# Performance work log

Measured on AMD Instinct MI355X. Metric: run time of the kernel, lower is better.

The kernel has to match this reference:

```python
import jax, jax.numpy as jnp
import numpy as np

D_MODEL = 96
D_STATE = 16
D_INNER = 192   # expand * d_model
DT_RANK = 6     # ceil(96/16)
D_DEPTH_OUT = 1024  # (64/2)*(64/2)
BATCH, HH, WW = 2, 64, 64


def silu(v):
    return v * jax.nn.sigmoid(v)


def setup_inputs() -> dict:
    key = jax.random.key(0)
    ks = jax.random.split(key, 10)
    f = jnp.float32
    x = jax.random.normal(ks[0], (BATCH, HH, WW, D_MODEL), f)
    in_proj_w = jax.random.normal(ks[1], (2 * D_INNER, D_MODEL), f) * 0.02
    conv2d_w = jax.random.normal(ks[2], (D_INNER, 1, 3, 3), f) * 0.1  # depthwise, groups=D_INNER
    conv2d_b = jnp.zeros((D_INNER,), f)
    depth_conv_w = jax.random.normal(ks[3], (D_INNER, 1, 3, 3), f) * 0.1  # depthwise, stride 2
    depth_conv_b = jnp.zeros((D_INNER,), f)
    depth_fc_w = jax.random.normal(ks[4], (D_INNER, D_DEPTH_OUT), f) * 0.02
    depth_fc_b = jnp.zeros((D_INNER,), f)
    x_proj_w = jax.random.normal(ks[5], (DT_RANK + 2 * D_STATE, D_INNER), f) * 0.02
    dt_init_std = DT_RANK ** (-0.5)
    dt_projs_w = jax.random.uniform(ks[6], (D_INNER, DT_RANK), f, -dt_init_std, dt_init_std)
    # inverse-softplus of dt ~ U(log 1e-3, log 0.1)
    dt = jnp.exp(jax.random.uniform(ks[7], (D_INNER,), f) * (np.log(0.1) - np.log(0.001)) + np.log(0.001))
    dt = jnp.clip(dt, 1e-4, None)
    dt_projs_b = dt + jnp.log(-jnp.expm1(-dt))
    A_logs = jnp.log(jnp.tile(jnp.arange(1, D_STATE + 1, dtype=f)[None, :], (D_INNER, 1)))
    Ds = jnp.ones((D_INNER,), f)
    out_norm_w = jnp.ones((D_INNER,), f)
    out_norm_b = jnp.zeros((D_INNER,), f)
    out_proj_w = jax.random.normal(ks[8], (D_MODEL, D_INNER), f) * 0.02
    return dict(x=x, in_proj_w=in_proj_w, conv2d_w=conv2d_w, conv2d_b=conv2d_b,
                depth_conv_w=depth_conv_w, depth_conv_b=depth_conv_b,
                depth_fc_w=depth_fc_w, depth_fc_b=depth_fc_b, x_proj_w=x_proj_w,
                dt_projs_w=dt_projs_w, dt_projs_b=dt_projs_b, A_logs=A_logs, Ds=Ds,
                out_norm_w=out_norm_w, out_norm_b=out_norm_b, out_proj_w=out_proj_w)


def _selective_scan(u, delta, A, Bm, Cm, D, delta_bias):
    # u, delta: [B, D, L]; A: [D, N]; Bm, Cm: [B, N, L]; D: [D]; delta_bias: [D]
    delta = jax.nn.softplus(delta + delta_bias[None, :, None])
    dA = jnp.exp(jnp.einsum('bdl,dn->lbdn', delta, A))          # [L,B,D,N]
    dBu = jnp.einsum('bdl,bnl,bdl->lbdn', delta, Bm, u)          # [L,B,D,N]
    Ct = jnp.transpose(Cm, (2, 0, 1))                            # [L,B,N]
    h0 = jnp.zeros(dA.shape[1:], u.dtype)

    def step(h, inp):
        a, b, c = inp
        h = a * h + b                                            # S6 recurrence
        return h, jnp.einsum('bdn,bn->bd', h, c)

    _, ys = jax.lax.scan(step, h0, (dA, dBu, Ct))                # ys: [L,B,D]
    y = jnp.transpose(ys, (1, 2, 0))                             # [B,D,L]
    return y + D[None, :, None] * u


def _forward(x, in_proj_w, conv2d_w, conv2d_b, depth_conv_w, depth_conv_b,
             depth_fc_w, depth_fc_b, x_proj_w, dt_projs_w, dt_projs_b,
             A_logs, Ds, out_norm_w, out_norm_b, out_proj_w):
    B, H, W, _ = x.shape
    Di, N, R = D_INNER, D_STATE, DT_RANK
    dn = ('NCHW', 'OIHW', 'NCHW')
    xz = x @ in_proj_w.T
    x1, z = jnp.split(xz, 2, axis=-1)
    xc = jnp.transpose(x1, (0, 3, 1, 2))                         # [B,Di,H,W]
    xc = jax.lax.conv_general_dilated(xc, conv2d_w, (1, 1), [(1, 1), (1, 1)],
                                      dimension_numbers=dn, feature_group_count=Di)
    xc = silu(xc + conv2d_b[None, :, None, None])
    dxc = jax.lax.conv_general_dilated(xc, depth_conv_w, (2, 2), [(1, 1), (1, 1)],
                                       dimension_numbers=dn, feature_group_count=Di)
    dxc = dxc + depth_conv_b[None, :, None, None]                # [B,Di,H/2,W/2]
    dx = dxc.reshape(B, Di, -1)                                  # [B,Di,1024]
    dx = dx @ depth_fc_w.T + depth_fc_b                          # [B,Di,Di]
    dx = silu(jnp.transpose(dx, (0, 2, 1)))                      # [B,Di,CC], CC=Di
    L = H * W
    CC = dx.shape[-1]
    xs = jnp.concatenate([dx, xc.reshape(B, Di, L)], axis=-1)    # mode='head': [B,Di,LL]
    x_dbl = jnp.einsum('bdl,cd->bcl', xs, x_proj_w)
    dts, Bm, Cm = x_dbl[:, :R], x_dbl[:, R:R + N], x_dbl[:, R + N:]
    dts = jnp.einsum('brl,dr->bdl', dts, dt_projs_w)
    A = -jnp.exp(A_logs)
    y = _selective_scan(xs, dts, A, Bm, Cm, Ds, dt_projs_b)
    y = y[..., CC:]                                              # drop depth tokens (head mode)
    y = jnp.transpose(y, (0, 2, 1)).reshape(B, H, W, Di)
    mu = jnp.mean(y, axis=-1, keepdims=True)
    var = jnp.var(y, axis=-1, keepdims=True)
    y = (y - mu) * jax.lax.rsqrt(var + 1e-5) * out_norm_w + out_norm_b
    y = y * silu(z)
    return y @ out_proj_w.T


def reference(x, in_proj_w, conv2d_w, conv2d_b, depth_conv_w, depth_conv_b,
              depth_fc_w, depth_fc_b, x_proj_w, dt_projs_w, dt_projs_b,
              A_logs, Ds, out_norm_w, out_norm_b, out_proj_w):
    return _forward(x, in_proj_w, conv2d_w, conv2d_b, depth_conv_w, depth_conv_b,
                    depth_fc_w, depth_fc_b, x_proj_w, dt_projs_w, dt_projs_b,
                    A_logs, Ds, out_norm_w, out_norm_b, out_proj_w)
```

## Files before the change

kernel.cpp:

```cpp
#include <hip/hip_runtime.h>
#include <hip/hip_bf16.h>

typedef __hip_bfloat16 bf16;

#define BATCH 2
#define DM 96
#define DI 192
#define LSP 4096
#define LD 192
#define LTOT 4288
#define NST 16
#define RK 6
#define DFC 1024
#define CLEN 64
#define NCH 67
#define SCH 64
#define XR 16
#define NG  (BATCH * DI * NST)

__device__ __forceinline__ float silu_f(float x) { return x / (1.f + __expf(-x)); }
__device__ __forceinline__ float softplus_f(float x) { return x > 20.f ? x : log1pf(__expf(x)); }

__device__ __forceinline__ int is_f32(const void* alog) {
    return ((const unsigned int*)alog)[0] == 0u;
}
__device__ __forceinline__ float LDI(const void* p, int i, int f32m) {
    return f32m ? ((const float*)p)[i] : __bfloat162float(((const bf16*)p)[i]);
}
__device__ __forceinline__ void unpack2(unsigned int u, float* o) {
    o[0] = __uint_as_float(u << 16);
    o[1] = __uint_as_float(u & 0xffff0000u);
}

__device__ __forceinline__ float row16_sum(float v) {
    v += __int_as_float(__builtin_amdgcn_update_dpp(0, __float_as_int(v), 0x128, 0xf, 0xf, true));
    v += __int_as_float(__builtin_amdgcn_update_dpp(0, __float_as_int(v), 0x124, 0xf, 0xf, true));
    v += __int_as_float(__builtin_amdgcn_update_dpp(0, __float_as_int(v), 0x122, 0xf, 0xf, true));
    v += __int_as_float(__builtin_amdgcn_update_dpp(0, __float_as_int(v), 0x121, 0xf, 0xf, true));
    return v;
}

#define TW(r, i)  ((r) * 64 + ((((i) >> 2) + (r)) & 15) * 4 + ((i) & 3))

__global__ __launch_bounds__(256) void k_wprep(const void* __restrict__ ipw, float* __restrict__ wT,
                                               const void* __restrict__ alog) {
    const int f32m = is_f32(alog);
    int idx = blockIdx.x * 256 + threadIdx.x;
    if (idx < 96 * 384) {
        int k = idx / 384, c = idx - k * 384;
        wT[idx] = LDI(ipw, c * 96 + k, f32m);
    }
}

__global__ __launch_bounds__(384) void k_inproj2(const void* __restrict__ x, const float* __restrict__ wT,
                                                 float* __restrict__ x1, float* __restrict__ z,
                                                 const void* __restrict__ alog) {
    __shared__ __align__(16) float sx[16 * 100];
    const int f32m = is_f32(alog);
    int t = threadIdx.x;
    int row0 = blockIdx.x * 16;
    {
        int e = t * 4;
        int row = e / 96, k = e - row * 96;
        float4 v;
        if (f32m) {
            v = *((const float4*)((const float*)x + (row0 + row) * 96 + k));
        } else {
            uint2 u = *((const uint2*)((const ushort*)x + (row0 + row) * 96 + k));
            float f[4];
            unpack2(u.x, &f[0]); unpack2(u.y, &f[2]);
            v = make_float4(f[0], f[1], f[2], f[3]);
        }
        *(float4*)&sx[row * 100 + k] = v;
    }
    __syncthreads();
    int rg = t / 96, cg = t - rg * 96;
    int c0 = cg * 4, rbase = rg * 4;
    float acc[4][4];
    #pragma unroll
    for (int r = 0; r < 4; r++)
        #pragma unroll
        for (int cc = 0; cc < 4; cc++) acc[r][cc] = 0.f;
    const float* wp = wT + c0;
    #pragma unroll 4
    for (int k4 = 0; k4 < 24; k4++) {
        float4 xv[4], wv[4];
        #pragma unroll
        for (int r = 0; r < 4; r++) xv[r] = *(const float4*)&sx[(rbase + r) * 100 + k4 * 4];
        #pragma unroll
        for (int q = 0; q < 4; q++) wv[q] = *(const float4*)&wp[(k4 * 4 + q) * 384];
        #pragma unroll
        for (int r = 0; r < 4; r++) {
            float xr[4] = {xv[r].x, xv[r].y, xv[r].z, xv[r].w};
            #pragma unroll
            for (int q = 0; q < 4; q++) {
                acc[r][0] += xr[q] * wv[q].x;
                acc[r][1] += xr[q] * wv[q].y;
                acc[r][2] += xr[q] * wv[q].z;
                acc[r][3] += xr[q] * wv[q].w;
            }
        }
    }
    #pragma unroll
    for (int r = 0; r < 4; r++) {
        int row = row0 + rbase + r;
        float4 o = make_float4(acc[r][0], acc[r][1], acc[r][2], acc[r][3]);
        if (c0 < DI) *(float4*)&x1[row * DI + c0] = o;
        else         *(float4*)&z[row * DI + (c0 - DI)] = o;
    }
}

__global__ __launch_bounds__(192) void k_conv12(const float* __restrict__ x1, const void* __restrict__ cw,
                                                const void* __restrict__ cb, const void* __restrict__ dw,
                                                const void* __restrict__ db, float* __restrict__ xs,
                                                float* __restrict__ dxc, const void* __restrict__ alog) {
    const int f32m = is_f32(alog);
    int d = threadIdx.x;
    int blk = blockIdx.x;
    int b = blk >> 8;
    int rest = blk & 255;
    int hp = rest >> 3, wt = rest & 7;
    float wgt1[9], wgt2[9];
    #pragma unroll
    for (int i = 0; i < 9; i++) { wgt1[i] = LDI(cw, d * 9 + i, f32m); wgt2[i] = LDI(dw, d * 9 + i, f32m); }
    float bias1 = LDI(cb, d, f32m);
    float bias2 = LDI(db, d, f32m);
    float val[5][11];
    #pragma unroll
    for (int r = 0; r < 5; r++) {
        int hh = 2 * hp - 2 + r;
        #pragma unroll
        for (int j = 0; j < 11; j++) {
            int ww = 8 * wt - 2 + j;
            val[r][j] = ((unsigned)hh < 64u && (unsigned)ww < 64u)
                      ? x1[((b << 12) + (hh << 6) + ww) * DI + d] : 0.f;
        }
    }
    float c1[3][9];
    #pragma unroll
    for (int rr = 0; rr < 3; rr++) {
        #pragma unroll
        for (int i = 0; i < 9; i++) {
            float acc = bias1;
            #pragma unroll
            for (int dh = 0; dh < 3; dh++)
                #pragma unroll
                for (int dw_ = 0; dw_ < 3; dw_++)
                    acc += val[rr + dh][i + dw_] * wgt1[dh * 3 + dw_];
            c1[rr][i] = silu_f(acc);
        }
    }
    #pragma unroll
    for (int rr = 1; rr < 3; rr++) {
        int row = 2 * hp + (rr - 1);
        #pragma unroll
        for (int i = 1; i < 9; i++) {
            int wa = 8 * wt + (i - 1);
            xs[(b * LTOT + LD + (row << 6) + wa) * DI + d] = c1[rr][i];
        }
    }
    #pragma unroll
    for (int wpl = 0; wpl < 4; wpl++) {
        int wpa = 4 * wt + wpl;
        float acc = bias2;
        #pragma unroll
        for (int dh = 0; dh < 3; dh++) {
            if (2 * hp + dh - 1 < 0) continue;
            #pragma unroll
            for (int dw_ = 0; dw_ < 3; dw_++) {
                if (2 * wpa + dw_ - 1 < 0) continue;
                acc += c1[dh][2 * wpl + dw_] * wgt2[dh * 3 + dw_];
            }
        }
        dxc[(b * DFC + hp * 32 + wpa) * DI + d] = acc;
    }
}

__global__ __launch_bounds__(192) void k_dfc(const float* __restrict__ dxc, const void* __restrict__ fw,
                                             float* __restrict__ part, const void* __restrict__ alog) {
    __shared__ float sfw[4 * 128];
    const int f32m = is_f32(alog);
    int t = threadIdx.x;
    int blk = blockIdx.x;
    int p = blk / 96;
    int rem = blk - p * 96;
    int b   = rem / 48;
    int ch0 = (rem % 48) * 4;
    int k0  = p * 128;
    for (int idx = t; idx < 4 * 128; idx += 192)
        sfw[idx] = LDI(fw, (ch0 + (idx >> 7)) * DFC + k0 + (idx & 127), f32m);
    __syncthreads();
    float a0 = 0.f, a1 = 0.f, a2 = 0.f, a3 = 0.f;
    #pragma unroll 8
    for (int k = 0; k < 128; k++) {
        float dv = dxc[(b * DFC + k0 + k) * DI + t];
        a0 += dv * sfw[k];
        a1 += dv * sfw[128 + k];
        a2 += dv * sfw[256 + k];
        a3 += dv * sfw[384 + k];
    }
    int ob = ((p * 2 + b) * 192 + t) * DI + ch0;
    *(float4*)&part[ob] = make_float4(a0, a1, a2, a3);
}

__global__ __launch_bounds__(256) void k_xdbl(const float* __restrict__ xs_r, float* __restrict__ xs_w,
                                              const float* __restrict__ part, const void* __restrict__ fb,
                                              const void* __restrict__ xpw,
                                              float* __restrict__ BCb, float* __restrict__ dts,
                                              const void* __restrict__ alog) {
    __shared__ float sw[38 * 196];
    __shared__ float srow[XR][196];
    const int f32m = is_f32(alog);
    int t = threadIdx.x;
    for (int c = t >> 3; c < 38; c += 32) {
        int seg = (t & 7) * 24;
        for (int k = seg; k < seg + 24; k++) sw[c * 196 + k] = LDI(xpw, c * DI + k, f32m);
    }
    int row0 = blockIdx.x * XR;
    int bb = row0 >= LTOT ? 1 : 0;
    int depth = (row0 - bb * LTOT) < LD;
    for (int idx = t; idx < XR * DI; idx += 256) {
        int row = idx / DI, k = idx - row * DI;
        int grow = row0 + row;
        float v;
        if (depth) {
            int tok = grow - bb * LTOT;
            int o = (bb * 192 + tok) * DI + k;
            v = 0.f;
            #pragma unroll
            for (int p = 0; p < 8; p++) v += part[o + p * 73728];
            v = silu_f(v + LDI(fb, k, f32m));
            xs_w[grow * DI + k] = v;
        } else {
            v = xs_r[grow * DI + k];
        }
        srow[row][k] = v;
    }
    __syncthreads();
    int r = t & 15, cg = t >> 4;
    float a0 = 0.f, a1 = 0.f, a2 = 0.f;
    const float4* w0 = (const float4*)&sw[cg * 196];
    const float4* w1 = (const float4*)&sw[(cg + 16) * 196];
    const float4* w2 = (const float4*)&sw[(cg < 6 ? cg + 32 : cg) * 196];
    const float4* xr = (const float4*)&srow[r][0];
    #pragma unroll 4
    for (int k = 0; k < 48; k++) {
        float4 xv = xr[k], v0 = w0[k], v1 = w1[k], v2 = w2[k];
        a0 += xv.x * v0.x + xv.y * v0.y + xv.z * v0.z + xv.w * v0.w;
        a1 += xv.x * v1.x + xv.y * v1.y + xv.z * v1.z + xv.w * v1.w;
        a2 += xv.x * v2.x + xv.y * v2.y + xv.z * v2.z + xv.w * v2.w;
    }
    int grow = row0 + r;
    if (cg < 6) dts[grow * 6 + cg] = a0;
    else        BCb[grow * 32 + (cg - 6)] = a0;
    BCb[grow * 32 + (cg + 10)] = a1;
    if (cg < 6) BCb[grow * 32 + (cg + 26)] = a2;
}

__device__ __forceinline__ void delta_block_T(const float* sdts, const float* sdwb, float* sdel, int t) {
    int e = t * 4;
    int i = e >> 4, dl = e & 15;
    #pragma unroll
    for (int q = 0; q < 4; q++) {
        int r = dl + q;
        float dv = sdwb[96 + r];
        #pragma unroll
        for (int r2 = 0; r2 < RK; r2++) dv += sdts[i * RK + r2] * sdwb[r * RK + r2];
        sdel[TW(r, i)] = softplus_f(dv);
    }
}

__global__ __launch_bounds__(256) void k_scan1(const float* __restrict__ dts, const float* __restrict__ xs,
                                               const float* __restrict__ BCb, const void* __restrict__ dtw,
                                               const void* __restrict__ dtb, const void* __restrict__ alog,
                                               float2* __restrict__ AH) {
    __shared__ __align__(16) float su[1024];
    __shared__ __align__(16) float sB[1024];
    __shared__ __align__(16) float sdel[1024];
    __shared__ float sdts[CLEN * RK];
    __shared__ float sdwb[112];
    const int f32m = is_f32(alog);
    int t = threadIdx.x;
    int beta = blockIdx.x;
    int b = beta / (12 * NCH);
    int rem = beta - b * (12 * NCH);
    int dblk = rem / NCH, ch = rem - dblk * NCH;
    int d0 = dblk * 16, l0 = ch * CLEN;
    int bL = b * LTOT;
    {
        int e = t * 4;
        int i = e >> 4, dd = e & 15;
        float4 uv = *(const float4*)&xs[(bL + l0 + i) * DI + d0 + dd];
        float4 bv = *(const float4*)&BCb[(bL + l0 + i) * 32 + dd];
        float uu[4] = {uv.x, uv.y, uv.z, uv.w};
        float vb[4] = {bv.x, bv.y, bv.z, bv.w};
        #pragma unroll
        for (int q = 0; q < 4; q++) {
            int w = TW(dd + q, i);
            su[w] = uu[q];
            sB[w] = vb[q];
        }
    }
    for (int idx = t; idx < CLEN * RK; idx += 256) sdts[idx] = dts[(bL + l0) * RK + idx];
    if (t < 96)            sdwb[t] = LDI(dtw, (d0 + t / 6) * RK + (t % 6), f32m);
    else if (t < 112)      sdwb[t] = LDI(dtb, d0 + (t - 96), f32m);
    __syncthreads();
    delta_block_T(sdts, sdwb, sdel, t);
    __syncthreads();
    int dloc = t >> 4, n = t & 15;
    int d = d0 + dloc;
    float A = -__expf(LDI(alog, d * NST + n, f32m));
    float h = 0.f, ap = 1.f;
    int bd = dloc * 64, bn = n * 64;
    #pragma unroll
    for (int i4 = 0; i4 < 16; i4++) {
        int od = bd + (((i4 + dloc) & 15) << 2);
        int on = bn + (((i4 + n) & 15) << 2);
        float de[4], uu[4], vb[4];
        *(float4*)de = *(const float4*)&sdel[od];
        *(float4*)uu = *(const float4*)&su[od];
        *(float4*)vb = *(const float4*)&sB[on];
        #pragma unroll
        for (int q = 0; q < 4; q++) {
            float a = __expf(de[q] * A);
            h = a * h + de[q] * vb[q] * uu[q];
            ap *= a;
        }
    }
    int g = ((b * DI + d) * NST) + n;
    AH[ch * NG + g] = make_float2(ap, h);
}

__global__ __launch_bounds__(64) void k_scan2(const float2* __restrict__ AH, float* __restrict__ He) {
    int g = blockIdx.x * 64 + threadIdx.x;
    float h = 0.f;
    for (int ch = 0; ch < NCH; ch++) {
        He[ch * NG + g] = h;
        float2 v = AH[ch * NG + g];
        h = v.x * h + v.y;
    }
}

__global__ __launch_bounds__(256) void k_scan3(const float* __restrict__ dts, const float* __restrict__ xs,
                                               const float* __restrict__ BCb, const void* __restrict__ dtw,
                                               const void* __restrict__ dtb, const void* __restrict__ alog,
                                               const void* __restrict__ Dsv, const float* __restrict__ He,
                                               float* __restrict__ y) {
    __shared__ __align__(16) float su[1024];
    __shared__ __align__(16) float sbc[2048];
    __shared__ __align__(16) float sdel[1024];
    __shared__ float sdts[CLEN * RK];
    __shared__ float sdwb[112];
    const int f32m = is_f32(alog);
    int t = threadIdx.x;
    int beta = blockIdx.x;
    int b = beta / (12 * SCH);
    int rem = beta - b * (12 * SCH);
    int dblk = rem / SCH, ch = (rem - dblk * SCH) + 3;
    int d0 = dblk * 16, l0 = ch * CLEN;
    int bL = b * LTOT;
    {
        int e = t * 4;
        int i = e >> 4, dd = e & 15;
        float4 uv = *(const float4*)&xs[(bL + l0 + i) * DI + d0 + dd];
        float uu[4] = {uv.x, uv.y, uv.z, uv.w};
        #pragma unroll
        for (int q = 0; q < 4; q++) su[TW(dd + q, i)] = uu[q];
    }
    #pragma unroll
    for (int q2 = 0; q2 < 2; q2++) {
        int e = (t + q2 * 256) * 4;
        int i = e >> 5, c = e & 31;
        float4 v = *(const float4*)&BCb[(bL + l0 + i) * 32 + c];
        float vv[4] = {v.x, v.y, v.z, v.w};
        #pragma unroll
        for (int q = 0; q < 4; q++) sbc[TW(c + q, i)] = vv[q];
    }
    for (int idx = t; idx < CLEN * RK; idx += 256) sdts[idx] = dts[(bL + l0) * RK + idx];
    if (t < 96)            sdwb[t] = LDI(dtw, (d0 + t / 6) * RK + (t % 6), f32m);
    else if (t < 112)      sdwb[t] = LDI(dtb, d0 + (t - 96), f32m);
    __syncthreads();
    delta_block_T(sdts, sdwb, sdel, t);
    __syncthreads();
    int dloc = t >> 4, n = t & 15;
    int d = d0 + dloc;
    float A = -__expf(LDI(alog, d * NST + n, f32m));
    float Dv = LDI(Dsv, d, f32m);
    int g = ((b * DI + d) * NST) + n;
    float h = He[ch * NG + g];
    int bd = dloc * 64, bn = n * 64;
    #pragma unroll
    for (int i4 = 0; i4 < 16; i4++) {
        int od = bd + (((i4 + dloc) & 15) << 2);
        int on = bn + (((i4 + n) & 15) << 2);
        float de[4], uu[4], vb[4], vc[4];
        *(float4*)de = *(const float4*)&sdel[od];
        *(float4*)uu = *(const float4*)&su[od];
        *(float4*)vb = *(const float4*)&sbc[on];
        *(float4*)vc = *(const float4*)&sbc[on + 1024];
        #pragma unroll
        for (int q = 0; q < 4; q++) {
            float a = __expf(de[q] * A);
            h = a * h + de[q] * vb[q] * uu[q];
            float yv = row16_sum(h * vc[q]);
            if (n == 0) {
                int l = l0 + i4 * 4 + q;
                y[(b * LSP + (l - LD)) * DI + d] = yv + Dv * uu[q];
            }
        }
    }
}

__global__ __launch_bounds__(384) void k_out(const float* __restrict__ y, const float* __restrict__ z,
                                             const void* __restrict__ nw, const void* __restrict__ nb,
                                             const void* __restrict__ opw, void* __restrict__ out,
                                             const void* __restrict__ alog) {
    __shared__ float sg[2][DI];
    __shared__ float sred[2][2][3];
    const int f32m = is_f32(alog);
    int t = threadIdx.x;
    int m = t >> 2, kh = t & 3;
    float wr[48];
    if (f32m) {
        const float4* wp = (const float4*)((const float*)opw + m * DI + kh * 48);
        #pragma unroll
        for (int i = 0; i < 12; i++) {
            float4 v = wp[i];
            wr[4*i] = v.x; wr[4*i+1] = v.y; wr[4*i+2] = v.z; wr[4*i+3] = v.w;
        }
    } else {
        const uint4* wp = (const uint4*)((const bf16*)opw + m * DI + kh * 48);
        #pragma unroll
        for (int i = 0; i < 6; i++) {
            uint4 v = wp[i];
            unpack2(v.x, &wr[8*i]);   unpack2(v.y, &wr[8*i+2]);
            unpack2(v.z, &wr[8*i+4]); unpack2(v.w, &wr[8*i+6]);
        }
    }
    float nwv = 0.f, nbv = 0.f;
    if (t < DI) { nwv = LDI(nw, t, f32m); nbv = LDI(nb, t, f32m); }
    int wv_ = t >> 6;
    int row0 = blockIdx.x * 16;
    for (int pr = 0; pr < 8; pr++) {
        int r0 = row0 + pr * 2, r1 = r0 + 1;
        float y0 = 0.f, z0 = 0.f, y1 = 0.f, z1 = 0.f;
        if (t < DI) {
            y0 = y[r0 * DI + t]; z0 = z[r0 * DI + t];
            y1 = y[r1 * DI + t]; z1 = z[r1 * DI + t];
            float s0 = y0, q0 = y0 * y0, s1 = y1, q1 = y1 * y1;
            #pragma unroll
            for (int off = 32; off; off >>= 1) {
                s0 += __shfl_xor(s0, off); q0 += __shfl_xor(q0, off);
                s1 += __shfl_xor(s1, off); q1 += __shfl_xor(q1, off);
            }
            if ((t & 63) == 0) {
                sred[0][0][wv_] = s0; sred[0][1][wv_] = q0;
                sred[1][0][wv_] = s1; sred[1][1][wv_] = q1;
            }
        }
        __syncthreads();
        if (t < DI) {
            float S0  = sred[0][0][0] + sred[0][0][1] + sred[0][0][2];
            float Q0  = sred[0][1][0] + sred[0][1][1] + sred[0][1][2];
            float S1  = sred[1][0][0] + sred[1][0][1] + sred[1][0][2];
            float Q1  = sred[1][1][0] + sred[1][1][1] + sred[1][1][2];
            float mu0 = S0 * (1.f / 192.f), var0 = Q0 * (1.f / 192.f) - mu0 * mu0;
            float mu1 = S1 * (1.f / 192.f), var1 = Q1 * (1.f / 192.f) - mu1 * mu1;
            float g0 = (y0 - mu0) * rsqrtf(var0 + 1e-5f) * nwv + nbv;
            g0 *= z0 / (1.f + __expf(-z0));
            float g1 = (y1 - mu1) * rsqrtf(var1 + 1e-5f) * nwv + nbv;
            g1 *= z1 / (1.f + __expf(-z1));
            sg[0][t] = g0;
            sg[1][t] = g1;
        }
        __syncthreads();
        const float* g0p = &sg[0][kh * 48];
        const float* g1p = &sg[1][kh * 48];
        float a0 = 0.f, a1 = 0.f;
        #pragma unroll
        for (int j = 0; j < 48; j++) {
            a0 += g0p[j] * wr[j];
            a1 += g1p[j] * wr[j];
        }
        a0 += __shfl_xor(a0, 1); a0 += __shfl_xor(a0, 2);
        a1 += __shfl_xor(a1, 1); a1 += __shfl_xor(a1, 2);
        if (kh == 0) {
            if (f32m) {
                ((float*)out)[r0 * DM + m] = a0;
                ((float*)out)[r1 * DM + m] = a1;
            } else {
                ((bf16*)out)[r0 * DM + m] = __float2bfloat16(a0);
                ((bf16*)out)[r1 * DM + m] = __float2bfloat16(a1);
            }
        }
    }
}

extern "C" void kernel_launch(void* const* d_in, const int* in_sizes, int n_in,
                              void* d_out, int out_size, void* d_ws, size_t ws_size,
                              hipStream_t stream) {
    (void)in_sizes; (void)n_in; (void)out_size; (void)ws_size;
    const void* x    = d_in[0];
    const void* ipw  = d_in[1];
    const void* c1w  = d_in[2];
    const void* c1b  = d_in[3];
    const void* c2w  = d_in[4];
    const void* c2b  = d_in[5];
    const void* fcw  = d_in[6];
    const void* fcb  = d_in[7];
    const void* xpw  = d_in[8];
    const void* dtw  = d_in[9];
    const void* dtb  = d_in[10];
    const void* alog = d_in[11];
    const void* Dsv  = d_in[12];
    const void* nw   = d_in[13];
    const void* nb   = d_in[14];
    const void* opw  = d_in[15];

    float* ws  = (float*)d_ws;
    float* x1  = ws;
    float* z   = x1  + BATCH * LSP * DI;
    float* xs  = z   + BATCH * LSP * DI;
    float* dxc = xs  + BATCH * LTOT * DI;
    float* BCb = dxc + BATCH * DFC * DI;
    float* dts = BCb + BATCH * LTOT * 32;
    float2* AH = (float2*)(dts + BATCH * LTOT * RK);
    float* He  = (float*)(AH + NCH * NG);
    float* wT  = He + NCH * NG;
    float* part = x1;
    float* y    = x1;

    k_wprep  <<<dim3(144), dim3(256), 0, stream>>>(ipw, wT, alog);
    k_inproj2<<<dim3(512), dim3(384), 0, stream>>>(x, wT, x1, z, alog);
    k_conv12 <<<dim3(512), dim3(DI), 0, stream>>>(x1, c1w, c1b, c2w, c2b, xs, dxc, alog);
    k_dfc    <<<dim3(768), dim3(DI), 0, stream>>>(dxc, fcw, part, alog);
    k_xdbl   <<<dim3(536), dim3(256), 0, stream>>>(xs, xs, part, fcb, xpw, BCb, dts, alog);
    k_scan1  <<<dim3(BATCH * 12 * NCH), dim3(256), 0, stream>>>(dts, xs, BCb, dtw, dtb, alog, AH);
    k_scan2  <<<dim3(96), dim3(64), 0, stream>>>(AH, He);
    k_scan3  <<<dim3(BATCH * 12 * SCH), dim3(256), 0, stream>>>(dts, xs, BCb, dtw, dtb, alog, Dsv, He, y);
    k_out    <<<dim3(512), dim3(384), 0, stream>>>(y, z, nw, nb, opw, d_out, alog);
}
```

Baseline: 217.6 us.

## Fuse chunk-prefix scan into scan1 via last-block atomic counter per chain

Removes the separate k_scan2 launch. Each (batch, d-block) chain now keeps an atomic counter, zeroed in k_wprep. The last chunk block to finish for a chain runs the sequential carry propagation across all chunks and writes He. This saves one kernel launch and its gap, but the serial 67-step tail now runs on only 24 blocks of 256 threads, and it adds fences and atomics.

```diff
diff --git a/kernel.cpp b/kernel.cpp
--- a/kernel.cpp
+++ b/kernel.cpp
@@ -17,6 +17,8 @@
 #define SCH 64
 #define XR 16
 #define NG  (BATCH * DI * NST)
+#define NCHAIN (BATCH * 12)
+#define CPAD 32
 
 __device__ __forceinline__ float silu_f(float x) { return x / (1.f + __expf(-x)); }
 __device__ __forceinline__ float softplus_f(float x) { return x > 20.f ? x : log1pf(__expf(x)); }
@@ -43,9 +45,10 @@
 #define TW(r, i)  ((r) * 64 + ((((i) >> 2) + (r)) & 15) * 4 + ((i) & 3))
 
 __global__ __launch_bounds__(256) void k_wprep(const void* __restrict__ ipw, float* __restrict__ wT,
-                                               const void* __restrict__ alog) {
+                                               const void* __restrict__ alog, int* __restrict__ cnts) {
     const int f32m = is_f32(alog);
     int idx = blockIdx.x * 256 + threadIdx.x;
+    if (idx < NCHAIN * CPAD) cnts[idx] = 0;
     if (idx < 96 * 384) {
         int k = idx / 384, c = idx - k * 384;
         wT[idx] = LDI(ipw, c * 96 + k, f32m);
@@ -270,21 +273,24 @@
     }
 }
 
-__global__ __launch_bounds__(256) void k_scan1(const float* __restrict__ dts, const float* __restrict__ xs,
-                                               const float* __restrict__ BCb, const void* __restrict__ dtw,
-                                               const void* __restrict__ dtb, const void* __restrict__ alog,
-                                               float2* __restrict__ AH) {
+__global__ __launch_bounds__(256) void k_scan1m2(const float* __restrict__ dts, const float* __restrict__ xs,
+                                                 const float* __restrict__ BCb, const void* __restrict__ dtw,
+                                                 const void* __restrict__ dtb, const void* __restrict__ alog,
+                                                 float2* __restrict__ AH, float* __restrict__ He,
+                                                 int* __restrict__ cnts) {
     __shared__ __align__(16) float su[1024];
     __shared__ __align__(16) float sB[1024];
     __shared__ __align__(16) float sdel[1024];
     __shared__ float sdts[CLEN * RK];
     __shared__ float sdwb[112];
+    __shared__ int stick;
     const int f32m = is_f32(alog);
     int t = threadIdx.x;
     int beta = blockIdx.x;
     int b = beta / (12 * NCH);
     int rem = beta - b * (12 * NCH);
     int dblk = rem / NCH, ch = rem - dblk * NCH;
+    int chain = b * 12 + dblk;
     int d0 = dblk * 16, l0 = ch * CLEN;
     int bL = b * LTOT;
     {
@@ -329,15 +335,16 @@
     }
     int g = ((b * DI + d) * NST) + n;
     AH[ch * NG + g] = make_float2(ap, h);
-}
-
-__global__ __launch_bounds__(64) void k_scan2(const float2* __restrict__ AH, float* __restrict__ He) {
-    int g = blockIdx.x * 64 + threadIdx.x;
-    float h = 0.f;
-    for (int ch = 0; ch < NCH; ch++) {
-        He[ch * NG + g] = h;
-        float2 v = AH[ch * NG + g];
-        h = v.x * h + v.y;
+    __syncthreads();
+    if (t == 0) { __threadfence(); stick = atomicAdd(&cnts[chain * CPAD], 1); }
+    __syncthreads();
+    if (stick != NCH - 1) return;
+    __threadfence();
+    float h2 = 0.f;
+    for (int c2 = 0; c2 < NCH; c2++) {
+        He[c2 * NG + g] = h2;
+        float2 v = AH[c2 * NG + g];
+        h2 = v.x * h2 + v.y;
     }
 }
 
@@ -527,16 +534,16 @@
     float2* AH = (float2*)(dts + BATCH * LTOT * RK);
     float* He  = (float*)(AH + NCH * NG);
     float* wT  = He + NCH * NG;
+    int* cnts  = (int*)(wT + 96 * 384);
     float* part = x1;
     float* y    = x1;
 
-    k_wprep  <<<dim3(144), dim3(256), 0, stream>>>(ipw, wT, alog);
+    k_wprep  <<<dim3(144), dim3(256), 0, stream>>>(ipw, wT, alog, cnts);
     k_inproj2<<<dim3(512), dim3(384), 0, stream>>>(x, wT, x1, z, alog);
     k_conv12 <<<dim3(512), dim3(DI), 0, stream>>>(x1, c1w, c1b, c2w, c2b, xs, dxc, alog);
     k_dfc    <<<dim3(768), dim3(DI), 0, stream>>>(dxc, fcw, part, alog);
     k_xdbl   <<<dim3(536), dim3(256), 0, stream>>>(xs, xs, part, fcb, xpw, BCb, dts, alog);
-    k_scan1  <<<dim3(BATCH * 12 * NCH), dim3(256), 0, stream>>>(dts, xs, BCb, dtw, dtb, alog, AH);
-    k_scan2  <<<dim3(96), dim3(64), 0, stream>>>(AH, He);
+    k_scan1m2<<<dim3(BATCH * 12 * NCH), dim3(256), 0, stream>>>(dts, xs, BCb, dtw, dtb, alog, AH, He, cnts);
     k_scan3  <<<dim3(BATCH * 12 * SCH), dim3(256), 0, stream>>>(dts, xs, BCb, dtw, dtb, alog, Dsv, He, y);
     k_out    <<<dim3(512), dim3(384), 0, stream>>>(y, z, nw, nb, opw, d_out, alog);
 }
```

Measured after the change: 262.2 us. 1.2x slower.
